# Kernel tuning notes

Measured on AMD Instinct MI355X. Metric: run time of the kernel, lower is better.

## Reference

```python
import jax, jax.numpy as jnp
import numpy as np

N = 25000      # nodes per type
E = 300000     # weight-edge rows
K = 16         # neighbors
F = 64         # in_feat
A = 64         # atten_dim
DW = 64        # weight_dim
CB = 8         # num_bit_conv
CV = 8         # num_vector_conv
OUT = 64       # out_feat
IN_K = CB * F + CV * (3 + 2 + 1)


def setup_inputs() -> dict:
    key = jax.random.key(0)
    ks = jax.random.split(key, 40)
    s = 0.05
    d = {}
    d['eu'] = jax.random.normal(ks[0], (N, F), jnp.float32)
    d['ei'] = jax.random.normal(ks[1], (N, F), jnp.float32)
    d['et'] = jax.random.normal(ks[2], (N, F), jnp.float32)
    d['ew'] = jax.random.normal(ks[3], (E, DW), jnp.float32)
    names = ['u_iw_j', 'u_tw_j', 'i_uw_j', 'i_tw_j', 't_uw_j', 't_iw_j']
    for i, nm in enumerate(names):
        d[nm] = jax.random.randint(ks[4 + i], (N, K), 0, N, jnp.int64 if jax.config.jax_enable_x64 else jnp.int32)
        d[nm.replace('_j', '_w')] = jax.random.randint(ks[10 + i], (N, K), 0, E, jnp.int64 if jax.config.jax_enable_x64 else jnp.int32)
    # per-type Attention1 params: user, item, tag
    for i, t in enumerate(['user', 'item', 'tag']):
        b = 16 + 4 * i
        d[f'W1_{t}'] = jax.random.normal(ks[b], (F + DW, A), jnp.float32) * s
        d[f'W2_{t}'] = jax.random.normal(ks[b + 1], (F, A), jnp.float32) * s
        d[f'b_{t}'] = jax.random.normal(ks[b + 2], (1, A), jnp.float32) * s
        d[f'v_{t}'] = jax.random.normal(ks[b + 3], (1, A), jnp.float32) * s
    d['U'] = jax.random.normal(ks[28], (F, A), jnp.float32) * s
    d['q'] = jax.random.normal(ks[29], (1, A), jnp.float32) * s
    d['p'] = jax.random.normal(ks[30], (1, A), jnp.float32) * s
    d['W_bit'] = jax.random.normal(ks[31], (CB, 3), jnp.float32) * s       # Conv2d(1,CB,(3,1))
    d['W_vec1'] = jax.random.normal(ks[32], (CV, 1, F), jnp.float32) * s   # Conv2d(1,CV,(1,F))
    d['W_vec2'] = jax.random.normal(ks[33], (CV, 2, F), jnp.float32) * s
    d['W_vec3'] = jax.random.normal(ks[34], (CV, 3, F), jnp.float32) * s
    d['Wf'] = jax.random.normal(ks[35], (IN_K, OUT), jnp.float32) * s
    d['bf'] = jax.random.normal(ks[36], (1, OUT), jnp.float32) * s
    return d


def _atten1(ev, ej, ew, v_j, v_w, W1, W2, b, v):
    ejp = jnp.concatenate([jnp.zeros((1, ej.shape[1]), ej.dtype), ej], axis=0)
    ewp = jnp.concatenate([jnp.zeros((1, ew.shape[1]), ew.dtype), ew], axis=0)
    eNj = ejp[v_j]                                  # [N,K,F]
    eNw = ewp[v_w]                                  # [N,K,DW]
    eNv = jnp.broadcast_to(ev[:, None, :], (ev.shape[0], v_j.shape[1], ev.shape[1]))
    eN_vw = jnp.concatenate([eNv, eNw], axis=-1)    # [N,K,F+DW]
    av = jnp.einsum('nkd,da->nka', eN_vw, W1) + jnp.einsum('nkf,fa->nka', eNj, W2) + b
    x = jax.nn.relu(av) @ v.T                       # [N,K,1]
    a = jax.nn.softmax(x, axis=1)
    return jnp.sum(a * eNj, axis=1)                 # [N,F]


def _atten2(u, i, t, U, q, p):
    uit = jnp.stack([u, i, t], axis=1)              # [N,3,F]
    x = jnp.einsum('nsf,fa->nsa', uit, U) + q
    x = jax.nn.relu(x) @ p.T                        # [N,3,1]
    b = jax.nn.softmax(x, axis=1)
    return b * uit                                  # [N,3,F]


def _conv(eN, W_bit, W_vec1, W_vec2, W_vec3):
    # eN: [N,3,F]
    bit = jax.nn.relu(jnp.einsum('njf,cj->ncf', eN, W_bit))       # [N,CB,F]
    bit = bit.reshape(bit.shape[0], -1)
    vec = []
    for j, W in ((1, W_vec1), (2, W_vec2), (3, W_vec3)):
        win = jnp.stack([eN[:, s:s + j, :] for s in range(3 - j + 1)], axis=1)  # [N,4-j,j,F]
        y = jax.nn.relu(jnp.einsum('nsjf,cjf->ncs', win, W))       # [N,CV,4-j]
        vec.append(y.reshape(y.shape[0], -1))
    return jnp.concatenate([bit] + vec, axis=1)                    # [N,IN_K]


def _forward(eu, ei, et, ew, params, idx):
    (W1u, W2u, bu, vu, W1i, W2i, bi, vi, W1t, W2t, bt, vt,
     U, q, p, W_bit, W_vec1, W_vec2, W_vec3, Wf, bf) = params
    (u_iw_j, u_iw_w, u_tw_j, u_tw_w, i_uw_j, i_uw_w,
     i_tw_j, i_tw_w, t_uw_j, t_uw_w, t_iw_j, t_iw_w) = idx
    eu_iN = _atten1(eu, ei, ew, u_iw_j, u_iw_w, W1i, W2i, bi, vi)
    eu_tN = _atten1(eu, et, ew, u_tw_j, u_tw_w, W1t, W2t, bt, vt)
    ei_uN = _atten1(ei, eu, ew, i_uw_j, i_uw_w, W1u, W2u, bu, vu)
    ei_tN = _atten1(ei, et, ew, i_tw_j, i_tw_w, W1t, W2t, bt, vt)
    et_uN = _atten1(et, eu, ew, t_uw_j, t_uw_w, W1u, W2u, bu, vu)
    et_iN = _atten1(et, ei, ew, t_iw_j, t_iw_w, W1i, W2i, bi, vi)
    euN = _atten2(eu, eu_iN, eu_tN, U, q, p)
    eiN = _atten2(ei_uN, ei, ei_tN, U, q, p)
    etN = _atten2(et_uN, et_iN, et, U, q, p)
    out = []
    for eN in (euN, eiN, etN):
        c = _conv(eN, W_bit, W_vec1, W_vec2, W_vec3)
        out.append(jax.nn.relu(c @ Wf + bf))
    return tuple(out)


def reference(eu, ei, et, ew,
              u_iw_j, u_iw_w, u_tw_j, u_tw_w, i_uw_j, i_uw_w, i_tw_j, i_tw_w,
              t_uw_j, t_uw_w, t_iw_j, t_iw_w,
              W1_user, W2_user, b_user, v_user,
              W1_item, W2_item, b_item, v_item,
              W1_tag, W2_tag, b_tag, v_tag,
              U, q, p, W_bit, W_vec1, W_vec2, W_vec3, Wf, bf):
    params = (W1_user, W2_user, b_user, v_user, W1_item, W2_item, b_item, v_item,
              W1_tag, W2_tag, b_tag, v_tag, U, q, p, W_bit, W_vec1, W_vec2, W_vec3, Wf, bf)
    idx = (u_iw_j, u_iw_w, u_tw_j, u_tw_w, i_uw_j, i_uw_w,
           i_tw_j, i_tw_w, t_uw_j, t_uw_w, t_iw_j, t_iw_w)
    return _forward(eu, ei, et, ew, params, idx)
```

## Files before the change

### kernel.cpp

```cpp
#include <hip/hip_runtime.h>
#include <math.h>

#define NN 25000
#define EE 300000
#define NT 1563
#define NT64 391
#define ET64 4688

typedef __attribute__((ext_vector_type(8))) short bf16x8;
typedef __attribute__((ext_vector_type(4))) float f32x4;
typedef __attribute__((ext_vector_type(2))) float f32x2;

__device__ __forceinline__ unsigned short f2bf(float f) {
    union { float f; unsigned u; } a; a.f = f;
    unsigned r = (a.u + 0x7fffu + ((a.u >> 16) & 1u)) >> 16;
    return (unsigned short)r;
}
__device__ __forceinline__ unsigned pack2(float lo, float hi) {
    return (unsigned)f2bf(lo) | ((unsigned)f2bf(hi) << 16);
}
__device__ __forceinline__ float bflo(unsigned p) {
    union { unsigned u; float f; } a; a.u = p << 16; return a.f;
}
__device__ __forceinline__ float bfhi(unsigned p) {
    union { unsigned u; float f; } a; a.u = p & 0xffff0000u; return a.f;
}
__device__ __forceinline__ unsigned packfp8x4(float a, float b, float c, float d) {
    int v = __builtin_amdgcn_cvt_pk_fp8_f32(a, b, 0, 0);
    v = __builtin_amdgcn_cvt_pk_fp8_f32(c, d, v, 1);
    return (unsigned)v;
}

__global__ __launch_bounds__(256) void head_kernel(
    const float* __restrict__ ew,
    const float* __restrict__ eu, const float* __restrict__ ei, const float* __restrict__ et,
    const float* __restrict__ W1u, const float* __restrict__ W1i, const float* __restrict__ W1t,
    const float* __restrict__ W2u, const float* __restrict__ W2i, const float* __restrict__ W2t,
    const float* __restrict__ bu, const float* __restrict__ bi, const float* __restrict__ bt,
    unsigned char* __restrict__ gw8, unsigned* __restrict__ preB,
    unsigned char* __restrict__ JG)
{
    __shared__ __align__(16) unsigned short stA[64 * 72];
    __shared__ __align__(16) float cS[64 * 68];
    const int t = threadIdx.x;
    const int lane = t & 63, wv = t >> 6;
    const int l15 = lane & 15, quad = lane >> 4;
    const int cw = wv * 16 + l15;
    const int bx = blockIdx.x;

    if (bx < ET64) {
        const float* Ws[3] = { W1u + 4096, W1i + 4096, W1t + 4096 };
        bf16x8 bf[3][2];
        #pragma unroll
        for (int w = 0; w < 3; ++w)
            #pragma unroll
            for (int ks = 0; ks < 2; ++ks)
                #pragma unroll
                for (int j = 0; j < 8; ++j)
                    bf[w][ks][j] = (short)f2bf(Ws[w][(ks * 32 + quad * 8 + j) * 64 + cw]);

        const int rowBase = bx * 64;
        #pragma unroll
        for (int i = 0; i < 4; ++i) {
            int idx = t + i * 256;
            int row = idx >> 4, cg = idx & 15;
            int gr = rowBase + row;
            float4 v4 = (gr < EE) ? *(const float4*)(ew + (size_t)gr * 64 + cg * 4)
                                  : make_float4(0.f, 0.f, 0.f, 0.f);
            uint2 pk = { pack2(v4.x, v4.y), pack2(v4.z, v4.w) };
            *(uint2*)&stA[row * 72 + cg * 4] = pk;
        }
        __syncthreads();
        bf16x8 af[4][2];
        #pragma unroll
        for (int m = 0; m < 4; ++m)
            #pragma unroll
            for (int ks = 0; ks < 2; ++ks)
                af[m][ks] = *(const bf16x8*)&stA[(m * 16 + l15) * 72 + ks * 32 + quad * 8];

        #pragma unroll
        for (int w = 0; w < 3; ++w) {
            if (w) __syncthreads();
            f32x4 acc[4];
            #pragma unroll
            for (int m = 0; m < 4; ++m) {
                acc[m].x = 0; acc[m].y = 0; acc[m].z = 0; acc[m].w = 0;
                #pragma unroll
                for (int ks = 0; ks < 2; ++ks)
                    acc[m] = __builtin_amdgcn_mfma_f32_16x16x32_bf16(af[m][ks], bf[w][ks], acc[m], 0, 0, 0);
                #pragma unroll
                for (int r = 0; r < 4; ++r)
                    cS[(m * 16 + quad * 4 + r) * 68 + cw] = acc[m][r];
            }
            __syncthreads();
            unsigned char* outg = gw8 + (size_t)w * EE * 64;
            #pragma unroll
            for (int i = 0; i < 2; ++i) {
                int task = t + i * 256;
                int row = task >> 3, seg = task & 7;
                int gr = rowBase + row;
                if (gr < EE) {
                    float4 a = *(const float4*)&cS[row * 68 + seg * 8];
                    float4 b = *(const float4*)&cS[row * 68 + seg * 8 + 4];
                    uint2 pk = { packfp8x4(a.x, a.y, a.z, a.w),
                                 packfp8x4(b.x, b.y, b.z, b.w) };
                    *(uint2*)(outg + (size_t)gr * 64 + seg * 8) = pk;
                }
            }
        }
    } else {
        const int yy = bx - ET64;
        const int y = yy / NT64;
        const int rowBase = (yy - y * NT64) * 64;
        const float* X; const float* Wa; const float* Wb; const float* W2;
        const float* ba; const float* bb; int oa, ob;
        switch (y) {
            case 0:  X = eu; Wa = W1i; ba = bi; oa = 0; Wb = W1t; bb = bt; ob = 1; W2 = W2u; break;
            case 1:  X = ei; Wa = W1u; ba = bu; oa = 2; Wb = W1t; bb = bt; ob = 3; W2 = W2i; break;
            default: X = et; Wa = W1u; ba = bu; oa = 4; Wb = W1i; bb = bi; ob = 5; W2 = W2t; break;
        }
        const float* Ws[3] = { Wa, Wb, W2 };
        const float bias_cw[3] = { ba[cw], bb[cw], 0.f };
        bf16x8 bf[3][2];
        #pragma unroll
        for (int w = 0; w < 3; ++w)
            #pragma unroll
            for (int ks = 0; ks < 2; ++ks)
                #pragma unroll
                for (int j = 0; j < 8; ++j)
                    bf[w][ks][j] = (short)f2bf(Ws[w][(ks * 32 + quad * 8 + j) * 64 + cw]);

        #pragma unroll
        for (int i = 0; i < 4; ++i) {
            int idx = t + i * 256;
            int row = idx >> 4, cg = idx & 15;
            int gr = rowBase + row;
            float4 v4 = (gr < NN) ? *(const float4*)(X + (size_t)gr * 64 + cg * 4)
                                  : make_float4(0.f, 0.f, 0.f, 0.f);
            uint2 pk = { pack2(v4.x, v4.y), pack2(v4.z, v4.w) };
            *(uint2*)&stA[row * 72 + cg * 4] = pk;
        }
        __syncthreads();
        bf16x8 af[4][2];
        #pragma unroll
        for (int m = 0; m < 4; ++m)
            #pragma unroll
            for (int ks = 0; ks < 2; ++ks)
                af[m][ks] = *(const bf16x8*)&stA[(m * 16 + l15) * 72 + ks * 32 + quad * 8];

        #pragma unroll
        for (int w = 0; w < 3; ++w) {
            if (w) __syncthreads();
            f32x4 acc[4];
            #pragma unroll
            for (int m = 0; m < 4; ++m) {
                acc[m].x = 0; acc[m].y = 0; acc[m].z = 0; acc[m].w = 0;
                #pragma unroll
                for (int ks = 0; ks < 2; ++ks)
                    acc[m] = __builtin_amdgcn_mfma_f32_16x16x32_bf16(af[m][ks], bf[w][ks], acc[m], 0, 0, 0);
                #pragma unroll
                for (int r = 0; r < 4; ++r)
                    cS[(m * 16 + quad * 4 + r) * 68 + cw] = acc[m][r] + bias_cw[w];
            }
            __syncthreads();
            #pragma unroll
            for (int i = 0; i < 2; ++i) {
                int task = t + i * 256;
                int row = task >> 3, seg = task & 7;
                int gr = rowBase + row;
                if (gr >= NN) continue;
                float4 a = *(const float4*)&cS[row * 68 + seg * 8];
                float4 b = *(const float4*)&cS[row * 68 + seg * 8 + 4];
                if (w < 2) {
                    int oi = (w == 0) ? oa : ob;
                    uint4 pk = { pack2(a.x, a.y), pack2(a.z, a.w),
                                 pack2(b.x, b.y), pack2(b.z, b.w) };
                    *(uint4*)(preB + ((size_t)oi * NN + gr) * 32 + seg * 4) = pk;
                } else {
                    unsigned char* dst = JG + ((size_t)y * NN + gr) * 192;
                    uint2 gj = { packfp8x4(a.x, a.y, a.z, a.w),
                                 packfp8x4(b.x, b.y, b.z, b.w) };
                    *(uint2*)(dst + seg * 8) = gj;
                    uint4 ej = *(const uint4*)&stA[row * 72 + seg * 8];
                    *(uint4*)(dst + 64 + seg * 16) = ej;
                }
            }
        }
    }
}

__global__ __launch_bounds__(256) void atten1_kernel(
    const unsigned* __restrict__ preB, const unsigned char* __restrict__ gw8,
    const unsigned char* __restrict__ JG,
    const float* __restrict__ vu, const float* __restrict__ vi, const float* __restrict__ vt,
    const int* __restrict__ u_iw_j, const int* __restrict__ u_iw_w,
    const int* __restrict__ u_tw_j, const int* __restrict__ u_tw_w,
    const int* __restrict__ i_uw_j, const int* __restrict__ i_uw_w,
    const int* __restrict__ i_tw_j, const int* __restrict__ i_tw_w,
    const int* __restrict__ t_uw_j, const int* __restrict__ t_uw_w,
    const int* __restrict__ t_iw_j, const int* __restrict__ t_iw_w,
    unsigned* __restrict__ aoB)
{
    const int y = blockIdx.y;
    const int* Vj; const int* Vw; const float* v; int g;
    switch (y) {
        case 0:  Vj = u_iw_j; Vw = u_iw_w; v = vi; g = 1; break;
        case 1:  Vj = u_tw_j; Vw = u_tw_w; v = vt; g = 2; break;
        case 2:  Vj = i_uw_j; Vw = i_uw_w; v = vu; g = 0; break;
        case 3:  Vj = i_tw_j; Vw = i_tw_w; v = vt; g = 2; break;
        case 4:  Vj = t_uw_j; Vw = t_uw_w; v = vu; g = 0; break;
        default: Vj = t_iw_j; Vw = t_iw_w; v = vi; g = 1; break;
    }
    const unsigned* pre = preB + (size_t)y * NN * 32;
    const unsigned char* gw = gw8 + (size_t)g * EE * 64;
    const unsigned char* jg = JG + (size_t)g * NN * 192;
    unsigned*            out = aoB + (size_t)y * NN * 32;

    const int lane = threadIdx.x & 63;
    const int n = blockIdx.x * 4 + (threadIdx.x >> 6);
    const int half = lane >> 5, pl = lane & 31;

    unsigned prep = pre[(size_t)n * 32 + pl];
    const float p0 = bflo(prep), p1 = bfhi(prep);
    const float2 vp = ((const float2*)v)[pl];

    float xk[8]; unsigned ejp[8];
    #pragma unroll
    for (int i = 0; i < 8; ++i) {
        int k = 2 * i + half;
        int w = Vw[n * 16 + k];
        int j = Vj[n * 16 + k];
        unsigned short gp = 0, jp = 0; unsigned ev = 0;
        if (w > 0) gp = *(const unsigned short*)(gw + (size_t)(w - 1) * 64 + pl * 2);
        if (j > 0) {
            const unsigned char* r = jg + (size_t)(j - 1) * 192;
            jp = *(const unsigned short*)(r + pl * 2);
            ev = *(const unsigned*)(r + 64 + pl * 4);
        }
        ejp[i] = ev;
        f32x2 g2 = __builtin_amdgcn_cvt_pk_f32_fp8((int)gp, false);
        f32x2 j2 = __builtin_amdgcn_cvt_pk_f32_fp8((int)jp, false);
        float x = fmaxf(p0 + g2.x + j2.x, 0.f) * vp.x
                + fmaxf(p1 + g2.y + j2.y, 0.f) * vp.y;
        x += __shfl_xor(x, 1, 64);  x += __shfl_xor(x, 2, 64);
        x += __shfl_xor(x, 4, 64);  x += __shfl_xor(x, 8, 64);
        x += __shfl_xor(x, 16, 64);
        xk[i] = x;
    }
    float m = xk[0];
    #pragma unroll
    for (int i = 1; i < 8; ++i) m = fmaxf(m, xk[i]);
    m = fmaxf(m, __shfl_xor(m, 32, 64));
    float s = 0.f;
    #pragma unroll
    for (int i = 0; i < 8; ++i) { xk[i] = __expf(xk[i] - m); s += xk[i]; }
    s += __shfl_xor(s, 32, 64);
    const float inv = 1.f / s;
    float a0 = 0.f, a1 = 0.f;
    #pragma unroll
    for (int i = 0; i < 8; ++i) {
        float wgt = xk[i] * inv;
        a0 = fmaf(wgt, bflo(ejp[i]), a0);
        a1 = fmaf(wgt, bfhi(ejp[i]), a1);
    }
    a0 += __shfl_xor(a0, 32, 64);
    a1 += __shfl_xor(a1, 32, 64);
    if (half == 0) out[(size_t)n * 32 + pl] = pack2(a0, a1);
}

__global__ __launch_bounds__(256, 3) void tail_kernel(
    const float* __restrict__ eu, const float* __restrict__ ei, const float* __restrict__ et,
    const unsigned* __restrict__ aoB,
    const float* __restrict__ U, const float* __restrict__ q, const float* __restrict__ p,
    const float* __restrict__ Wbit, const float* __restrict__ Wv1,
    const float* __restrict__ Wv2, const float* __restrict__ Wv3,
    const float* __restrict__ Wf, const float* __restrict__ bfv,
    float* __restrict__ out)
{
    __shared__ __align__(16) unsigned short uitA[48 * 72];
    __shared__ __align__(16) unsigned short eNA[48 * 72];
    __shared__ __align__(16) unsigned short wcf[6 * 64 * 8];
    __shared__ __align__(16) unsigned short c_sh[16 * 584];
    __shared__ float G_sh[48 * 52];
    __shared__ float xpart[4 * 48];
    __shared__ float bcoef[16 * 4];

    const int t = threadIdx.x;
    const int lane = t & 63;
    const int wv = t >> 6;
    const int l15 = lane & 15;
    const int quad = lane >> 4;
    const int type = blockIdx.y;
    const float* xf = (type == 0) ? eu : (type == 1) ? ei : et;
    const int cw = wv * 16 + l15;
    const float qv = q[cw], pv = p[cw], bfb = bfv[cw];

    float wb[8][3];
    #pragma unroll
    for (int c = 0; c < 8; ++c)
        #pragma unroll
        for (int s = 0; s < 3; ++s) wb[c][s] = Wbit[c * 3 + s];

    bf16x8 ufrag[2];
    #pragma unroll
    for (int ks = 0; ks < 2; ++ks)
        #pragma unroll
        for (int j = 0; j < 8; ++j) {
            int f = ks * 32 + quad * 8 + j;
            ufrag[ks][j] = (short)f2bf(U[f * 64 + cw]);
        }
    bf16x8 wff[18];
    #pragma unroll
    for (int ks = 0; ks < 18; ++ks)
        #pragma unroll
        for (int j = 0; j < 8; ++j) {
            int k = ks * 32 + quad * 8 + j;
            float w = (k < 560) ? Wf[(size_t)k * 64 + cw] : 0.f;
            wff[ks][j] = (short)f2bf(w);
        }
    for (int slot = t; slot < 384; slot += 256) {
        int fi = slot >> 6, l = slot & 63;
        int nt_ = fi >> 1, ks = fi & 1;
        int r = nt_ * 16 + (l & 15);
        unsigned short vals[8];
        #pragma unroll
        for (int j = 0; j < 8; ++j) {
            int f = ks * 32 + (l >> 4) * 8 + j;
            float wv_;
            if (r < 8)       wv_ = Wv1[r * 64 + f];
            else if (r < 24) { int u = r - 8;  wv_ = Wv2[(u >> 1) * 128 + (u & 1) * 64 + f]; }
            else             { int u = r - 24; wv_ = Wv3[(u / 3) * 192 + (u % 3) * 64 + f]; }
            vals[j] = f2bf(wv_);
        }
        uint4 pk = { (unsigned)vals[0] | ((unsigned)vals[1] << 16),
                     (unsigned)vals[2] | ((unsigned)vals[3] << 16),
                     (unsigned)vals[4] | ((unsigned)vals[5] << 16),
                     (unsigned)vals[6] | ((unsigned)vals[7] << 16) };
        *(uint4*)&wcf[slot * 8] = pk;
    }

    for (int tile = blockIdx.x; tile < NT; tile += gridDim.x) {
        const int nodeBase = tile * 16;
        __syncthreads();
        #pragma unroll
        for (int i = 0; i < 3; ++i) {
            int idx = t + i * 256;
            int row = idx >> 4, cg = idx & 15;
            int nl = row / 3, s = row - nl * 3;
            int n = nodeBase + nl;
            uint2 pk;
            if (s == type) {
                float4 v4 = (n < NN) ? *(const float4*)(xf + (size_t)n * 64 + cg * 4)
                                     : make_float4(0.f, 0.f, 0.f, 0.f);
                pk.x = pack2(v4.x, v4.y); pk.y = pack2(v4.z, v4.w);
            } else {
                int aoidx = (type == 0) ? (s - 1)
                          : (type == 1) ? ((s == 0) ? 2 : 3)
                                        : ((s == 0) ? 4 : 5);
                pk = (n < NN) ? *(const uint2*)(aoB + ((size_t)aoidx * NN + n) * 32 + cg * 2)
                              : make_uint2(0u, 0u);
            }
            *(uint2*)&uitA[row * 72 + cg * 4] = pk;
        }
        __syncthreads();
        {
            f32x4 av[3];
            #pragma unroll
            for (int mt = 0; mt < 3; ++mt) { av[mt].x = 0; av[mt].y = 0; av[mt].z = 0; av[mt].w = 0; }
            #pragma unroll
            for (int mt = 0; mt < 3; ++mt)
                #pragma unroll
                for (int ks = 0; ks < 2; ++ks) {
                    bf16x8 a = *(const bf16x8*)&uitA[(mt * 16 + l15) * 72 + ks * 32 + quad * 8];
                    av[mt] = __builtin_amdgcn_mfma_f32_16x16x32_bf16(a, ufrag[ks], av[mt], 0, 0, 0);
                }
            #pragma unroll
            for (int mt = 0; mt < 3; ++mt)
                #pragma unroll
                for (int r = 0; r < 4; ++r) {
                    float val = fmaxf(av[mt][r] + qv, 0.f) * pv;
                    val += __shfl_xor(val, 1, 64); val += __shfl_xor(val, 2, 64);
                    val += __shfl_xor(val, 4, 64); val += __shfl_xor(val, 8, 64);
                    if (l15 == 0) xpart[wv * 48 + mt * 16 + quad * 4 + r] = val;
                }
        }
        __syncthreads();
        if (t < 16) {
            float xv[3];
            #pragma unroll
            for (int s = 0; s < 3; ++s)
                xv[s] = xpart[t * 3 + s] + xpart[48 + t * 3 + s]
                      + xpart[96 + t * 3 + s] + xpart[144 + t * 3 + s];
            float mm = fmaxf(xv[0], fmaxf(xv[1], xv[2]));
            float e0 = __expf(xv[0] - mm), e1 = __expf(xv[1] - mm), e2 = __expf(xv[2] - mm);
            float inv = 1.f / (e0 + e1 + e2);
            bcoef[t * 4 + 0] = e0 * inv; bcoef[t * 4 + 1] = e1 * inv; bcoef[t * 4 + 2] = e2 * inv;
        }
        __syncthreads();
        #pragma unroll
        for (int i = 0; i < 2; ++i) {
            int task = t + i * 256;
            int nl = task >> 5, fp = task & 31;
            float b0 = bcoef[nl * 4], b1 = bcoef[nl * 4 + 1], b2 = bcoef[nl * 4 + 2];
            unsigned u0 = *(const unsigned*)&uitA[(nl * 3 + 0) * 72 + fp * 2];
            unsigned u1 = *(const unsigned*)&uitA[(nl * 3 + 1) * 72 + fp * 2];
            unsigned u2 = *(const unsigned*)&uitA[(nl * 3 + 2) * 72 + fp * 2];
            float e0l = b0 * bflo(u0), e0h = b0 * bfhi(u0);
            float e1l = b1 * bflo(u1), e1h = b1 * bfhi(u1);
            float e2l = b2 * bflo(u2), e2h = b2 * bfhi(u2);
            *(unsigned*)&eNA[(nl * 3 + 0) * 72 + fp * 2] = pack2(e0l, e0h);
            *(unsigned*)&eNA[(nl * 3 + 1) * 72 + fp * 2] = pack2(e1l, e1h);
            *(unsigned*)&eNA[(nl * 3 + 2) * 72 + fp * 2] = pack2(e2l, e2h);
            #pragma unroll
            for (int c = 0; c < 8; ++c) {
                float lo = fmaxf(wb[c][0] * e0l + wb[c][1] * e1l + wb[c][2] * e2l, 0.f);
                float hi = fmaxf(wb[c][0] * e0h + wb[c][1] * e1h + wb[c][2] * e2h, 0.f);
                *(unsigned*)&c_sh[nl * 584 + c * 64 + fp * 2] = pack2(lo, hi);
            }
        }
        __syncthreads();
        #pragma unroll
        for (int pi = 0; pi < 3; ++pi) {
            int pr = wv + pi * 4;
            if (pr < 9) {
                int mm = pr / 3, nn_ = pr - mm * 3;
                f32x4 g; g.x = 0; g.y = 0; g.z = 0; g.w = 0;
                #pragma unroll
                for (int ks = 0; ks < 2; ++ks) {
                    bf16x8 a = *(const bf16x8*)&eNA[(mm * 16 + l15) * 72 + ks * 32 + quad * 8];
                    bf16x8 b = *(const bf16x8*)&wcf[((nn_ * 2 + ks) * 64 + lane) * 8];
                    g = __builtin_amdgcn_mfma_f32_16x16x32_bf16(a, b, g, 0, 0, 0);
                }
                #pragma unroll
                for (int r = 0; r < 4; ++r)
                    G_sh[(mm * 16 + quad * 4 + r) * 52 + nn_ * 16 + l15] = g[r];
            }
        }
        __syncthreads();
        #pragma unroll
        for (int i = 0; i < 4; ++i) {
            int task = t + i * 256;
            int vvv = task >> 4, nl = task & 15;
            unsigned short res = 0;
            if (vvv < 24) {
                int c = vvv / 3, s = vvv - c * 3;
                res = f2bf(fmaxf(G_sh[(nl * 3 + s) * 52 + c], 0.f));
            } else if (vvv < 40) {
                int u = vvv - 24, c = u >> 1, s = u & 1;
                float val = G_sh[(nl * 3 + s) * 52 + 8 + 2 * c]
                          + G_sh[(nl * 3 + s + 1) * 52 + 8 + 2 * c + 1];
                res = f2bf(fmaxf(val, 0.f));
            } else if (vvv < 48) {
                int c = vvv - 40;
                float val = G_sh[(nl * 3 + 0) * 52 + 24 + 3 * c]
                          + G_sh[(nl * 3 + 1) * 52 + 24 + 3 * c + 1]
                          + G_sh[(nl * 3 + 2) * 52 + 24 + 3 * c + 2];
                res = f2bf(fmaxf(val, 0.f));
            }
            c_sh[nl * 584 + 512 + vvv] = res;
        }
        __syncthreads();
        {
            f32x4 acc; acc.x = 0; acc.y = 0; acc.z = 0; acc.w = 0;
            const unsigned short* ap = &c_sh[l15 * 584 + quad * 8];
            #pragma unroll
            for (int ks = 0; ks < 18; ++ks) {
                bf16x8 a = *(const bf16x8*)(ap + ks * 32);
                acc = __builtin_amdgcn_mfma_f32_16x16x32_bf16(a, wff[ks], acc, 0, 0, 0);
            }
            float* outT = out + (size_t)type * NN * 64;
            #pragma unroll
            for (int r = 0; r < 4; ++r) {
                int node = nodeBase + quad * 4 + r;
                if (node < NN) outT[(size_t)node * 64 + cw] = fmaxf(acc[r] + bfb, 0.f);
            }
        }
    }
}

extern "C" void kernel_launch(void* const* d_in, const int* in_sizes, int n_in,
                              void* d_out, int out_size, void* d_ws, size_t ws_size,
                              hipStream_t stream)
{
    const float* eu = (const float*)d_in[0];
    const float* ei = (const float*)d_in[1];
    const float* et = (const float*)d_in[2];
    const float* ew = (const float*)d_in[3];
    const int* u_iw_j = (const int*)d_in[4];
    const int* u_iw_w = (const int*)d_in[5];
    const int* u_tw_j = (const int*)d_in[6];
    const int* u_tw_w = (const int*)d_in[7];
    const int* i_uw_j = (const int*)d_in[8];
    const int* i_uw_w = (const int*)d_in[9];
    const int* i_tw_j = (const int*)d_in[10];
    const int* i_tw_w = (const int*)d_in[11];
    const int* t_uw_j = (const int*)d_in[12];
    const int* t_uw_w = (const int*)d_in[13];
    const int* t_iw_j = (const int*)d_in[14];
    const int* t_iw_w = (const int*)d_in[15];
    const float* W1_user = (const float*)d_in[16];
    const float* W2_user = (const float*)d_in[17];
    const float* b_user  = (const float*)d_in[18];
    const float* v_user  = (const float*)d_in[19];
    const float* W1_item = (const float*)d_in[20];
    const float* W2_item = (const float*)d_in[21];
    const float* b_item  = (const float*)d_in[22];
    const float* v_item  = (const float*)d_in[23];
    const float* W1_tag  = (const float*)d_in[24];
    const float* W2_tag  = (const float*)d_in[25];
    const float* b_tag   = (const float*)d_in[26];
    const float* v_tag   = (const float*)d_in[27];
    const float* U    = (const float*)d_in[28];
    const float* q    = (const float*)d_in[29];
    const float* p    = (const float*)d_in[30];
    const float* Wbit = (const float*)d_in[31];
    const float* Wv1  = (const float*)d_in[32];
    const float* Wv2  = (const float*)d_in[33];
    const float* Wv3  = (const float*)d_in[34];
    const float* Wf   = (const float*)d_in[35];
    const float* bfv  = (const float*)d_in[36];
    float* out = (float*)d_out;

    unsigned char* gw8 = (unsigned char*)d_ws;
    unsigned* preB = (unsigned*)(gw8 + (size_t)3 * EE * 64);
    unsigned char* JG = (unsigned char*)(preB + (size_t)6 * NN * 32);
    unsigned* aoB = (unsigned*)(JG + (size_t)3 * NN * 192);

    const dim3 blk(256);

    head_kernel<<<ET64 + 3 * NT64, blk, 0, stream>>>(
        ew, eu, ei, et,
        W1_user, W1_item, W1_tag, W2_user, W2_item, W2_tag,
        b_user, b_item, b_tag, gw8, preB, JG);

    atten1_kernel<<<dim3(NN / 4, 6), blk, 0, stream>>>(
        preB, gw8, JG, v_user, v_item, v_tag,
        u_iw_j, u_iw_w, u_tw_j, u_tw_w, i_uw_j, i_uw_w,
        i_tw_j, i_tw_w, t_uw_j, t_uw_w, t_iw_j, t_iw_w, aoB);

    tail_kernel<<<dim3(256, 3), blk, 0, stream>>>(
        eu, ei, et, aoB,
        U, q, p, Wbit, Wv1, Wv2, Wv3, Wf, bfv, out);
}
```

Baseline: 465.9 us.

## Add zero sentinel rows to gather tables and widen atten1 per-lane loads

```diff
diff --git a/kernel.cpp b/kernel.cpp
--- a/kernel.cpp
+++ b/kernel.cpp
@@ -49,6 +49,10 @@
     const int bx = blockIdx.x;
 
     if (bx < ET64) {
+        if (bx == 0 && t < 48) {
+            int w = t >> 4;
+            ((unsigned*)(gw8 + (size_t)w * (EE + 1) * 64))[t & 15] = 0u;
+        }
         const float* Ws[3] = { W1u + 4096, W1i + 4096, W1t + 4096 };
         bf16x8 bf[3][2];
         #pragma unroll
@@ -93,7 +97,7 @@
                     cS[(m * 16 + quad * 4 + r) * 68 + cw] = acc[m][r];
             }
             __syncthreads();
-            unsigned char* outg = gw8 + (size_t)w * EE * 64;
+            unsigned char* outg = gw8 + (size_t)w * (EE + 1) * 64 + 64;
             #pragma unroll
             for (int i = 0; i < 2; ++i) {
                 int task = t + i * 256;
@@ -112,6 +116,8 @@
         const int yy = bx - ET64;
         const int y = yy / NT64;
         const int rowBase = (yy - y * NT64) * 64;
+        if (rowBase == 0 && t < 48)
+            ((unsigned*)(JG + (size_t)y * (NN + 1) * 192))[t] = 0u;
         const float* X; const float* Wa; const float* Wb; const float* W2;
         const float* ba; const float* bb; int oa, ob;
         switch (y) {
@@ -177,7 +183,7 @@
                                  pack2(b.x, b.y), pack2(b.z, b.w) };
                     *(uint4*)(preB + ((size_t)oi * NN + gr) * 32 + seg * 4) = pk;
                 } else {
-                    unsigned char* dst = JG + ((size_t)y * NN + gr) * 192;
+                    unsigned char* dst = JG + ((size_t)y * (NN + 1) + gr + 1) * 192;
                     uint2 gj = { packfp8x4(a.x, a.y, a.z, a.w),
                                  packfp8x4(b.x, b.y, b.z, b.w) };
                     *(uint2*)(dst + seg * 8) = gj;
@@ -212,60 +218,79 @@
         default: Vj = t_iw_j; Vw = t_iw_w; v = vi; g = 1; break;
     }
     const unsigned* pre = preB + (size_t)y * NN * 32;
-    const unsigned char* gw = gw8 + (size_t)g * EE * 64;
-    const unsigned char* jg = JG + (size_t)g * NN * 192;
+    const unsigned char* gw = gw8 + (size_t)g * (EE + 1) * 64;
+    const unsigned char* jg = JG + (size_t)g * (NN + 1) * 192;
     unsigned*            out = aoB + (size_t)y * NN * 32;
 
     const int lane = threadIdx.x & 63;
     const int n = blockIdx.x * 4 + (threadIdx.x >> 6);
-    const int half = lane >> 5, pl = lane & 31;
-
-    unsigned prep = pre[(size_t)n * 32 + pl];
-    const float p0 = bflo(prep), p1 = bfhi(prep);
-    const float2 vp = ((const float2*)v)[pl];
-
-    float xk[8]; unsigned ejp[8];
-    #pragma unroll
-    for (int i = 0; i < 8; ++i) {
-        int k = 2 * i + half;
-        int w = Vw[n * 16 + k];
-        int j = Vj[n * 16 + k];
-        unsigned short gp = 0, jp = 0; unsigned ev = 0;
-        if (w > 0) gp = *(const unsigned short*)(gw + (size_t)(w - 1) * 64 + pl * 2);
-        if (j > 0) {
-            const unsigned char* r = jg + (size_t)(j - 1) * 192;
-            jp = *(const unsigned short*)(r + pl * 2);
-            ev = *(const unsigned*)(r + 64 + pl * 4);
-        }
-        ejp[i] = ev;
-        f32x2 g2 = __builtin_amdgcn_cvt_pk_f32_fp8((int)gp, false);
-        f32x2 j2 = __builtin_amdgcn_cvt_pk_f32_fp8((int)jp, false);
-        float x = fmaxf(p0 + g2.x + j2.x, 0.f) * vp.x
-                + fmaxf(p1 + g2.y + j2.y, 0.f) * vp.y;
-        x += __shfl_xor(x, 1, 64);  x += __shfl_xor(x, 2, 64);
-        x += __shfl_xor(x, 4, 64);  x += __shfl_xor(x, 8, 64);
-        x += __shfl_xor(x, 16, 64);
+    const int q = lane >> 4, r = lane & 15;
+
+    const uint2 prep = *(const uint2*)(pre + (size_t)n * 32 + 2 * r);
+    const float pf0 = bflo(prep.x), pf1 = bfhi(prep.x);
+    const float pf2 = bflo(prep.y), pf3 = bfhi(prep.y);
+    const float4 v4 = *(const float4*)(v + r * 4);
+
+    const int4 wi = *(const int4*)(Vw + n * 16 + q * 4);
+    const int4 ji = *(const int4*)(Vj + n * 16 + q * 4);
+    const int wid[4] = { wi.x, wi.y, wi.z, wi.w };
+    const int jid[4] = { ji.x, ji.y, ji.z, ji.w };
+
+    unsigned gwv[4], gjv[4]; uint2 ejv[4];
+    #pragma unroll
+    for (int i = 0; i < 4; ++i)
+        gwv[i] = *(const unsigned*)(gw + (size_t)wid[i] * 64 + r * 4);
+    #pragma unroll
+    for (int i = 0; i < 4; ++i) {
+        const unsigned char* row = jg + (size_t)jid[i] * 192;
+        gjv[i] = *(const unsigned*)(row + r * 4);
+        ejv[i] = *(const uint2*)(row + 64 + r * 8);
+    }
+
+    float xk[4];
+    #pragma unroll
+    for (int i = 0; i < 4; ++i) {
+        f32x2 g01 = __builtin_amdgcn_cvt_pk_f32_fp8((int)gwv[i], false);
+        f32x2 g23 = __builtin_amdgcn_cvt_pk_f32_fp8((int)gwv[i], true);
+        f32x2 j01 = __builtin_amdgcn_cvt_pk_f32_fp8((int)gjv[i], false);
+        f32x2 j23 = __builtin_amdgcn_cvt_pk_f32_fp8((int)gjv[i], true);
+        float x =          fmaxf(pf0 + g01.x + j01.x, 0.f) * v4.x;
+        x = fmaf(fmaxf(pf1 + g01.y + j01.y, 0.f), v4.y, x);
+        x = fmaf(fmaxf(pf2 + g23.x + j23.x, 0.f), v4.z, x);
+        x = fmaf(fmaxf(pf3 + g23.y + j23.y, 0.f), v4.w, x);
+        x += __shfl_xor(x, 1, 64);
+        x += __shfl_xor(x, 2, 64);
+        x += __shfl_xor(x, 4, 64);
+        x += __shfl_xor(x, 8, 64);
         xk[i] = x;
     }
-    float m = xk[0];
-    #pragma unroll
-    for (int i = 1; i < 8; ++i) m = fmaxf(m, xk[i]);
+    float m = fmaxf(fmaxf(xk[0], xk[1]), fmaxf(xk[2], xk[3]));
+    m = fmaxf(m, __shfl_xor(m, 16, 64));
     m = fmaxf(m, __shfl_xor(m, 32, 64));
-    float s = 0.f;
-    #pragma unroll
-    for (int i = 0; i < 8; ++i) { xk[i] = __expf(xk[i] - m); s += xk[i]; }
+    float e0 = __expf(xk[0] - m), e1 = __expf(xk[1] - m);
+    float e2 = __expf(xk[2] - m), e3 = __expf(xk[3] - m);
+    float s = (e0 + e1) + (e2 + e3);
+    s += __shfl_xor(s, 16, 64);
     s += __shfl_xor(s, 32, 64);
     const float inv = 1.f / s;
-    float a0 = 0.f, a1 = 0.f;
-    #pragma unroll
-    for (int i = 0; i < 8; ++i) {
-        float wgt = xk[i] * inv;
-        a0 = fmaf(wgt, bflo(ejp[i]), a0);
-        a1 = fmaf(wgt, bfhi(ejp[i]), a1);
-    }
-    a0 += __shfl_xor(a0, 32, 64);
-    a1 += __shfl_xor(a1, 32, 64);
-    if (half == 0) out[(size_t)n * 32 + pl] = pack2(a0, a1);
+
+    float a0 = 0.f, a1 = 0.f, a2 = 0.f, a3 = 0.f;
+    const float wgt[4] = { e0 * inv, e1 * inv, e2 * inv, e3 * inv };
+    #pragma unroll
+    for (int i = 0; i < 4; ++i) {
+        a0 = fmaf(wgt[i], bflo(ejv[i].x), a0);
+        a1 = fmaf(wgt[i], bfhi(ejv[i].x), a1);
+        a2 = fmaf(wgt[i], bflo(ejv[i].y), a2);
+        a3 = fmaf(wgt[i], bfhi(ejv[i].y), a3);
+    }
+    a0 += __shfl_xor(a0, 16, 64); a0 += __shfl_xor(a0, 32, 64);
+    a1 += __shfl_xor(a1, 16, 64); a1 += __shfl_xor(a1, 32, 64);
+    a2 += __shfl_xor(a2, 16, 64); a2 += __shfl_xor(a2, 32, 64);
+    a3 += __shfl_xor(a3, 16, 64); a3 += __shfl_xor(a3, 32, 64);
+    if (q == 0) {
+        uint2 pk = { pack2(a0, a1), pack2(a2, a3) };
+        *(uint2*)(out + (size_t)n * 32 + 2 * r) = pk;
+    }
 }
 
 __global__ __launch_bounds__(256, 3) void tail_kernel(
@@ -522,9 +547,9 @@
     float* out = (float*)d_out;
 
     unsigned char* gw8 = (unsigned char*)d_ws;
-    unsigned* preB = (unsigned*)(gw8 + (size_t)3 * EE * 64);
+    unsigned* preB = (unsigned*)(gw8 + (size_t)3 * (EE + 1) * 64);
     unsigned char* JG = (unsigned char*)(preB + (size_t)6 * NN * 32);
-    unsigned* aoB = (unsigned*)(JG + (size_t)3 * NN * 192);
+    unsigned* aoB = (unsigned*)(JG + (size_t)3 * (NN + 1) * 192);
 
     const dim3 blk(256);
 
```

Result: faster. 399.1 us (-14.3%).
